# Kernel optimization log

Measured on AMD Instinct MI355X. Metric: run time of the kernel, lower is better.

The kernel has to match this reference:

```python
import jax, jax.numpy as jnp
import numpy as np


def setup_inputs() -> dict:
    key = jax.random.key(0)
    ks = jax.random.split(key, 9)
    N, C, SY, SX = 256, 128, 11, 25
    DM, DC, D = 64, 64, 128
    return {
        "f_t_global": jax.random.normal(ks[0], (N, D), dtype=jnp.float32),
        "x_t_local": jax.random.normal(ks[1], (N, C, SY, SX), dtype=jnp.float32),
        "x_t_prev_local": jax.random.normal(ks[2], (N, C, SY, SX), dtype=jnp.float32),
        "m_t": jax.random.normal(ks[3], (N, DM), dtype=jnp.float32),
        "m_t_prev": jax.random.normal(ks[4], (N, DM), dtype=jnp.float32),
        "c_t": jax.random.normal(ks[5], (N, DC), dtype=jnp.float32),
        "c_t_prev": jax.random.normal(ks[6], (N, DC), dtype=jnp.float32),
        "W_join": jax.random.normal(ks[7], (C + DM + DC, D), dtype=jnp.float32) * 0.05,
        "b_join": jax.random.normal(ks[8], (D,), dtype=jnp.float32) * 0.05,
    }


def reference(f_t_global, x_t_local, x_t_prev_local, m_t, m_t_prev, c_t, c_t_prev, W_join, b_join):
    N, C, SY, SX = x_t_local.shape
    P = SY * SX
    DM = m_t.shape[1]
    # join_obs(local, m, c) = concat([local, m, c]) @ W_join + b_join, split for efficiency
    Wl = W_join[:C]                 # [C, D]
    Wm = W_join[C:C + DM]           # [DM, D]
    Wc = W_join[C + DM:]            # [DC, D]
    # [N, C, SY, SX] -> [P, N, C]: all spatial positions batched at once
    loc_t = x_t_local.reshape(N, C, P).transpose(2, 0, 1)
    loc_p = x_t_prev_local.reshape(N, C, P).transpose(2, 0, 1)
    bias_t = m_t @ Wm + c_t @ Wc + b_join             # [N, D], shared across positions
    bias_p = m_t_prev @ Wm + c_t_prev @ Wc + b_join   # [N, D]
    positive = jnp.einsum('pnc,cd->pnd', loc_p, Wl) + bias_p[None]  # [P, N, D]
    pred_loc = jnp.einsum('pnc,cd->pnd', loc_t, Wl) + bias_t[None]  # [P, N, D]

    # loss1: global prediction vs per-position prev-local positives
    logits1 = jnp.einsum('nd,pmd->pnm', f_t_global, positive)   # [P, N, N]
    # loss2: per-position current-local vs per-position prev-local
    logits2 = jnp.einsum('pnd,pmd->pnm', pred_loc, positive)    # [P, N, N]

    def mean_infonce(logits):
        # cross_entropy(logits, arange(N)) averaged over batch, then over positions
        lse = jax.nn.logsumexp(logits, axis=-1)            # [P, N]
        diag = jnp.diagonal(logits, axis1=1, axis2=2)      # [P, N]
        return jnp.mean(lse - diag)

    loss1 = mean_infonce(logits1)
    loss2 = mean_infonce(logits2)
    return loss1 + loss2
```

## Files before the change

kernel.cpp:

```cpp
#include <hip/hip_runtime.h>

#define Nn 256
#define Cc 128
#define Pp 275
#define Dd 128

typedef unsigned int u32;
typedef unsigned short u16;
typedef float f32x4 __attribute__((ext_vector_type(4)));
typedef short bf16x8 __attribute__((ext_vector_type(8)));

__device__ __forceinline__ float bf2f(u16 h) {
    return __uint_as_float(((u32)h) << 16);
}
__device__ __forceinline__ u16 f2bf(float f) {
    u32 u = __float_as_uint(f);
    return (u16)((u + 0x7fffu + ((u >> 16) & 1u)) >> 16);
}

__global__ __launch_bounds__(256) void bias_kernel(
    const float* __restrict__ m_t, const float* __restrict__ m_p,
    const float* __restrict__ c_t, const float* __restrict__ c_p,
    const float* __restrict__ W, const float* __restrict__ b,
    const float* __restrict__ f,
    float* __restrict__ bias_t, float* __restrict__ bias_p,
    u16* __restrict__ f_bf, u16* __restrict__ WlT)
{
    int idx = blockIdx.x * 256 + threadIdx.x;
    int n = idx >> 7, d = idx & 127;
    float at = 0.f, ap = 0.f;
#pragma unroll 8
    for (int k = 0; k < 64; ++k) {
        float wm = W[(128 + k) * 128 + d];
        float wc = W[(192 + k) * 128 + d];
        at = fmaf(m_t[n * 64 + k], wm, at);
        at = fmaf(c_t[n * 64 + k], wc, at);
        ap = fmaf(m_p[n * 64 + k], wm, ap);
        ap = fmaf(c_p[n * 64 + k], wc, ap);
    }
    float bb = b[d];
    bias_t[idx] = at + bb;
    bias_p[idx] = ap + bb;
    f_bf[idx] = f2bf(f[idx]);
    if (idx < 16384) {
        int dd = idx >> 7, cc = idx & 127;
        WlT[idx] = f2bf(W[cc * 128 + dd]);
    }
}

__global__ __launch_bounds__(512) void join_full_kernel(
    const float* __restrict__ x_t, const float* __restrict__ x_p,
    const u16* __restrict__ WlT,
    const float* __restrict__ bias_t, const float* __restrict__ bias_p,
    u16* __restrict__ pred, u16* __restrict__ pos)
{
    __shared__ u16 xlds[275 * 128];
    const int tid = threadIdx.x;
    const int pass = blockIdx.x;
    const int n = blockIdx.y;
    const int w = tid >> 6;
    const int l = tid & 63;
    const int g = l >> 4;

    const float* sx = (pass ? x_p : x_t) + (size_t)n * (Cc * Pp);
    u16* outp = pass ? pos : pred;

    bf16x8 B[4];
    {
        const int row = w * 16 + (l & 15);
#pragma unroll
        for (int kk = 0; kk < 4; ++kk)
            B[kk] = *reinterpret_cast<const bf16x8*>(
                (const char*)WlT + row * 256 + kk * 64 + g * 16);
    }
    const float bv = (pass ? bias_p : bias_t)[n * 128 + w * 16 + (l & 15)];

    {
        const int c0 = (tid >> 3) * 2;
        const int j = tid & 7;
        const float* r0p = sx + (size_t)c0 * Pp;
        const float* r1p = r0p + Pp;

        f32x4 v0[9], v1[9];
#pragma unroll
        for (int i = 0; i < 9; ++i) {
            const int q = j + 8 * i;
            if (q < 68) {
                v0[i] = *reinterpret_cast<const f32x4*>(r0p + 4 * q);
                v1[i] = *reinterpret_cast<const f32x4*>(r1p + 4 * q);
            } else if (q == 68) {
                f32x4 a, c;
#pragma unroll
                for (int e = 0; e < 4; ++e) {
                    int pe = 4 * 68 + e; if (pe > Pp - 1) pe = Pp - 1;
                    a[e] = r0p[pe]; c[e] = r1p[pe];
                }
                v0[i] = a; v1[i] = c;
            }
        }
        asm volatile("" ::: "memory");
#pragma unroll
        for (int i = 0; i < 9; ++i) {
            const int q = j + 8 * i;
            if (q < 69) {
#pragma unroll
                for (int e = 0; e < 4; ++e) {
                    int p = 4 * q + e; if (p > Pp - 1) p = Pp - 1;
                    const int col = (c0 * 2) ^ ((p & 7) << 4) ^ (((p >> 3) & 1) << 5);
                    *reinterpret_cast<u32*>((char*)xlds + p * 256 + col) =
                        (u32)f2bf(v0[i][e]) | ((u32)f2bf(v1[i][e]) << 16);
                }
            }
        }
    }
    __syncthreads();

    const int d = w * 16 + (l & 15);
#pragma unroll
    for (int t = 0; t < 18; ++t) {
        const int p0 = (t < 17) ? t * 16 : 259;
        const int arow = p0 + (l & 15);
        bf16x8 A[4];
#pragma unroll
        for (int kk = 0; kk < 4; ++kk) {
            const int col = (kk * 64 + g * 16) ^ ((arow & 7) << 4) ^ (((arow >> 3) & 1) << 5);
            A[kk] = *reinterpret_cast<const bf16x8*>((const char*)xlds + arow * 256 + col);
        }
        f32x4 acc = {0.f, 0.f, 0.f, 0.f};
#pragma unroll
        for (int kk = 0; kk < 4; ++kk)
            acc = __builtin_amdgcn_mfma_f32_16x16x32_bf16(A[kk], B[kk], acc, 0, 0, 0);
#pragma unroll
        for (int r = 0; r < 4; ++r) {
            const int p = p0 + g * 4 + r;
            outp[((size_t)p * Nn + n) * Dd + d] = f2bf(acc[r] + bv);
        }
    }
}

__global__ __launch_bounds__(512) void logits_part_kernel(
    const u16* __restrict__ f_bf,
    const u16* __restrict__ pred, const u16* __restrict__ pos,
    float* __restrict__ spart, float* __restrict__ dgarr)
{
    __shared__ u16 lds[128 * Dd];
    const int tid = threadIdx.x;
    const int sel = blockIdx.x >> 1;
    const int mhalf = blockIdx.x & 1;
    const int p = blockIdx.y;
    const int w = tid >> 6;
    const int l = tid & 63;
    const int r0 = w * 32;

    {
        const uint4* src = reinterpret_cast<const uint4*>(
            pos + (size_t)p * (Nn * Dd) + (size_t)mhalf * 128 * Dd);
#pragma unroll
        for (int it = 0; it < 4; ++it) {
            int j = tid + 512 * it;
            int row = j >> 4;
            int colb = (j & 15) << 4;
            uint4 v = src[j];
            *reinterpret_cast<uint4*>((char*)lds + row * 256 + (colb ^ ((row & 7) << 4))) = v;
        }
    }

    const u16* Abase = sel ? (pred + (size_t)p * (Nn * Dd)) : f_bf;
    bf16x8 A[2][4];
    {
        const int arow = l & 15;
        const int acol = (l >> 4) << 4;
#pragma unroll
        for (int rt = 0; rt < 2; ++rt)
#pragma unroll
            for (int kk = 0; kk < 4; ++kk) {
                const char* ap = (const char*)Abase
                               + (size_t)(r0 + rt * 16 + arow) * 256 + kk * 64 + acol;
                A[rt][kk] = *reinterpret_cast<const bf16x8*>(ap);
            }
    }

    __syncthreads();

    const float L2E = 1.4426950408889634f;
    float s_[2][4];
    float dg[2][4];
#pragma unroll
    for (int rt = 0; rt < 2; ++rt)
#pragma unroll
        for (int r = 0; r < 4; ++r) { s_[rt][r] = 0.f; dg[rt][r] = 0.f; }

    const int mcol = l & 15;
    const int bcol = (l >> 4) << 4;

    for (int ctl = 0; ctl < 8; ++ctl) {
        bf16x8 B[4];
        const int mrow = ctl * 16 + mcol;
#pragma unroll
        for (int kk = 0; kk < 4; ++kk) {
            int cb = kk * 64 + bcol;
            B[kk] = *reinterpret_cast<const bf16x8*>(
                (const char*)lds + mrow * 256 + (cb ^ ((mrow & 7) << 4)));
        }
#pragma unroll
        for (int rt = 0; rt < 2; ++rt) {
            f32x4 acc = {0.f, 0.f, 0.f, 0.f};
#pragma unroll
            for (int kk = 0; kk < 4; ++kk)
                acc = __builtin_amdgcn_mfma_f32_16x16x32_bf16(A[rt][kk], B[kk], acc, 0, 0, 0);
            const bool isdg_ct = ((mhalf * 8 + ctl) == ((r0 >> 4) + rt));
#pragma unroll
            for (int r = 0; r < 4; ++r) {
                float v = acc[r];
                s_[rt][r] += __builtin_amdgcn_exp2f(fmaf(v, L2E, -64.f));
                if (isdg_ct && ((l & 15) == (((l >> 4) << 2) + r))) dg[rt][r] = v;
            }
        }
    }

    float* sp = spart + (((size_t)(sel * Pp + p) * 2 + mhalf) << 8);
    float* dp = dgarr + (((size_t)(sel * Pp + p)) << 8);
    const bool owns_dg = ((w >> 2) == mhalf);
#pragma unroll
    for (int rt = 0; rt < 2; ++rt)
#pragma unroll
        for (int r = 0; r < 4; ++r) {
            float s = s_[rt][r];
            s += __shfl_xor(s, 1);
            s += __shfl_xor(s, 2);
            s += __shfl_xor(s, 4);
            s += __shfl_xor(s, 8);
            if ((l & 15) == (((l >> 4) << 2) + r)) {
                const int nn = r0 + rt * 16 + ((l >> 4) << 2) + r;
                sp[nn] = s;
                if (owns_dg) dp[nn] = dg[rt][r];
            }
        }
}

__global__ __launch_bounds__(256) void merge_kernel(
    const float* __restrict__ spart, const float* __restrict__ dgarr,
    float* __restrict__ partial)
{
    __shared__ float red[256];
    const int sel = blockIdx.x;
    const int p = blockIdx.y;
    const int n = threadIdx.x;
    const size_t base = ((size_t)(sel * Pp + p) * 2) << 8;
    float s = spart[base + n] + spart[base + 256 + n];
    float dgv = dgarr[(((size_t)(sel * Pp + p)) << 8) + n];
    float val = 0.6931471805599453f * (64.f + __log2f(s)) - dgv;
    red[n] = val;
    __syncthreads();
    for (int k = 128; k > 0; k >>= 1) {
        if (n < k) red[n] += red[n + k];
        __syncthreads();
    }
    if (n == 0) partial[sel * Pp + p] = red[0];
}

__global__ __launch_bounds__(256) void reduce_kernel(
    const float* __restrict__ partial, float* __restrict__ out)
{
    __shared__ float red[256];
    float s = 0.f;
    for (int i = threadIdx.x; i < 2 * Pp; i += 256) s += partial[i];
    red[threadIdx.x] = s;
    __syncthreads();
    for (int k = 128; k > 0; k >>= 1) {
        if (threadIdx.x < k) red[threadIdx.x] += red[threadIdx.x + k];
        __syncthreads();
    }
    if (threadIdx.x == 0) out[0] = red[0] * (1.0f / (Pp * (float)Nn));
}

extern "C" void kernel_launch(void* const* d_in, const int* in_sizes, int n_in,
                              void* d_out, int out_size, void* d_ws, size_t ws_size,
                              hipStream_t stream)
{
    const float* f   = (const float*)d_in[0];
    const float* x_t = (const float*)d_in[1];
    const float* x_p = (const float*)d_in[2];
    const float* m_t = (const float*)d_in[3];
    const float* m_p = (const float*)d_in[4];
    const float* c_t = (const float*)d_in[5];
    const float* c_p = (const float*)d_in[6];
    const float* W   = (const float*)d_in[7];
    const float* b   = (const float*)d_in[8];

    char* ws = (char*)d_ws;
    const size_t SLAB = (size_t)Pp * Nn * Dd;

    float* bias_t = (float*)ws;
    float* bias_p = bias_t + Nn * Dd;
    u16* f_bf = (u16*)(ws + 262144);
    u16* WlT  = f_bf + Nn * Dd;
    u16* pred = (u16*)(ws + 360448);
    u16* pos  = pred + SLAB;
    float* partial = (float*)(pos + SLAB);
    float* spart   = partial + 2 * Pp;
    float* dgarr   = spart + (size_t)2 * Pp * 2 * 256;

    bias_kernel<<<dim3(Nn * Dd / 256), 256, 0, stream>>>(m_t, m_p, c_t, c_p, W, b, f,
                                                         bias_t, bias_p, f_bf, WlT);
    join_full_kernel<<<dim3(2, Nn), 512, 0, stream>>>(x_t, x_p, WlT, bias_t, bias_p,
                                                      pred, pos);
    logits_part_kernel<<<dim3(4, Pp), 512, 0, stream>>>(f_bf, pred, pos, spart, dgarr);
    merge_kernel<<<dim3(2, Pp), 256, 0, stream>>>(spart, dgarr, partial);
    reduce_kernel<<<1, 256, 0, stream>>>(partial, (float*)d_out);
}
```

Measured before the change: 62.20 us.

## Split join kernel input staging into two halves to overlap loads with MFMA

The join kernel now stages the spatial positions in two LDS halves (144 and 131 positions). It issues the global loads for the second half into registers before running the MFMA tiles on the first half, so memory latency hides behind compute. LDS use stays about the same (two buffers of 144 rows) while register pressure rises from holding the prefetched second half. It also adds a second barrier.

```diff
diff --git a/kernel.cpp b/kernel.cpp
--- a/kernel.cpp
+++ b/kernel.cpp
@@ -48,13 +48,13 @@
     }
 }
 
-__global__ __launch_bounds__(512) void join_full_kernel(
+__global__ __launch_bounds__(512) void join_dbuf2_kernel(
     const float* __restrict__ x_t, const float* __restrict__ x_p,
     const u16* __restrict__ WlT,
     const float* __restrict__ bias_t, const float* __restrict__ bias_p,
     u16* __restrict__ pred, u16* __restrict__ pos)
 {
-    __shared__ u16 xlds[275 * 128];
+    __shared__ u16 xlds[2][144 * 128];
     const int tid = threadIdx.x;
     const int pass = blockIdx.x;
     const int n = blockIdx.y;
@@ -75,39 +75,32 @@
     }
     const float bv = (pass ? bias_p : bias_t)[n * 128 + w * 16 + (l & 15)];
 
+    const int c0 = (tid >> 3) * 2;
+    const int j = tid & 7;
+    const float* r0p = sx + (size_t)c0 * Pp;
+    const float* r1p = r0p + Pp;
+    const int d = w * 16 + (l & 15);
+
     {
-        const int c0 = (tid >> 3) * 2;
-        const int j = tid & 7;
-        const float* r0p = sx + (size_t)c0 * Pp;
-        const float* r1p = r0p + Pp;
-
-        f32x4 v0[9], v1[9];
-#pragma unroll
-        for (int i = 0; i < 9; ++i) {
+        f32x4 v0[5], v1[5];
+#pragma unroll
+        for (int i = 0; i < 5; ++i) {
             const int q = j + 8 * i;
-            if (q < 68) {
+            if (q < 36) {
                 v0[i] = *reinterpret_cast<const f32x4*>(r0p + 4 * q);
                 v1[i] = *reinterpret_cast<const f32x4*>(r1p + 4 * q);
-            } else if (q == 68) {
-                f32x4 a, c;
+            }
+        }
+        asm volatile("" ::: "memory");
+#pragma unroll
+        for (int i = 0; i < 5; ++i) {
+            const int q = j + 8 * i;
+            if (q < 36) {
 #pragma unroll
                 for (int e = 0; e < 4; ++e) {
-                    int pe = 4 * 68 + e; if (pe > Pp - 1) pe = Pp - 1;
-                    a[e] = r0p[pe]; c[e] = r1p[pe];
-                }
-                v0[i] = a; v1[i] = c;
-            }
-        }
-        asm volatile("" ::: "memory");
-#pragma unroll
-        for (int i = 0; i < 9; ++i) {
-            const int q = j + 8 * i;
-            if (q < 69) {
-#pragma unroll
-                for (int e = 0; e < 4; ++e) {
-                    int p = 4 * q + e; if (p > Pp - 1) p = Pp - 1;
-                    const int col = (c0 * 2) ^ ((p & 7) << 4) ^ (((p >> 3) & 1) << 5);
-                    *reinterpret_cast<u32*>((char*)xlds + p * 256 + col) =
+                    const int lp = 4 * q + e;
+                    const int col = (c0 * 2) ^ ((lp & 7) << 4) ^ (((lp >> 3) & 1) << 5);
+                    *reinterpret_cast<u32*>((char*)&xlds[0][0] + lp * 256 + col) =
                         (u32)f2bf(v0[i][e]) | ((u32)f2bf(v1[i][e]) << 16);
                 }
             }
@@ -115,16 +108,70 @@
     }
     __syncthreads();
 
-    const int d = w * 16 + (l & 15);
-#pragma unroll
-    for (int t = 0; t < 18; ++t) {
+    f32x4 u0[5], u1[5];
+#pragma unroll
+    for (int i = 0; i < 5; ++i) {
+        const int q = j + 8 * i;
+        if (q < 32) {
+            u0[i] = *reinterpret_cast<const f32x4*>(r0p + 144 + 4 * q);
+            u1[i] = *reinterpret_cast<const f32x4*>(r1p + 144 + 4 * q);
+        } else if (q == 32) {
+            f32x4 a, c;
+#pragma unroll
+            for (int e = 0; e < 4; ++e) {
+                int pe = 144 + 128 + e; if (pe > Pp - 1) pe = Pp - 1;
+                a[e] = r0p[pe]; c[e] = r1p[pe];
+            }
+            u0[i] = a; u1[i] = c;
+        }
+    }
+    asm volatile("" ::: "memory");
+
+#pragma unroll
+    for (int t = 0; t < 9; ++t) {
+        const int p0 = t * 16;
+        const int lrow = p0 + (l & 15);
+        bf16x8 A[4];
+#pragma unroll
+        for (int kk = 0; kk < 4; ++kk) {
+            const int col = (kk * 64 + g * 16) ^ ((lrow & 7) << 4) ^ (((lrow >> 3) & 1) << 5);
+            A[kk] = *reinterpret_cast<const bf16x8*>((const char*)&xlds[0][0] + lrow * 256 + col);
+        }
+        f32x4 acc = {0.f, 0.f, 0.f, 0.f};
+#pragma unroll
+        for (int kk = 0; kk < 4; ++kk)
+            acc = __builtin_amdgcn_mfma_f32_16x16x32_bf16(A[kk], B[kk], acc, 0, 0, 0);
+#pragma unroll
+        for (int r = 0; r < 4; ++r) {
+            const int p = p0 + g * 4 + r;
+            outp[((size_t)p * Nn + n) * Dd + d] = f2bf(acc[r] + bv);
+        }
+    }
+
+#pragma unroll
+    for (int i = 0; i < 5; ++i) {
+        const int q = j + 8 * i;
+        if (q < 33) {
+#pragma unroll
+            for (int e = 0; e < 4; ++e) {
+                const int lp = 4 * q + e;
+                const int col = (c0 * 2) ^ ((lp & 7) << 4) ^ (((lp >> 3) & 1) << 5);
+                *reinterpret_cast<u32*>((char*)&xlds[1][0] + lp * 256 + col) =
+                    (u32)f2bf(u0[i][e]) | ((u32)f2bf(u1[i][e]) << 16);
+            }
+        }
+    }
+    __syncthreads();
+
+#pragma unroll
+    for (int t = 9; t < 18; ++t) {
         const int p0 = (t < 17) ? t * 16 : 259;
-        const int arow = p0 + (l & 15);
+        const int lrow = p0 - 144 + (l & 15);
         bf16x8 A[4];
 #pragma unroll
         for (int kk = 0; kk < 4; ++kk) {
-            const int col = (kk * 64 + g * 16) ^ ((arow & 7) << 4) ^ (((arow >> 3) & 1) << 5);
-            A[kk] = *reinterpret_cast<const bf16x8*>((const char*)xlds + arow * 256 + col);
+            const int col = (kk * 64 + g * 16) ^ ((lrow & 7) << 4) ^ (((lrow >> 3) & 1) << 5);
+            A[kk] = *reinterpret_cast<const bf16x8*>((const char*)&xlds[1][0] + lrow * 256 + col);
         }
         f32x4 acc = {0.f, 0.f, 0.f, 0.f};
 #pragma unroll
@@ -303,8 +350,8 @@
 
     bias_kernel<<<dim3(Nn * Dd / 256), 256, 0, stream>>>(m_t, m_p, c_t, c_p, W, b, f,
                                                          bias_t, bias_p, f_bf, WlT);
-    join_full_kernel<<<dim3(2, Nn), 512, 0, stream>>>(x_t, x_p, WlT, bias_t, bias_p,
-                                                      pred, pos);
+    join_dbuf2_kernel<<<dim3(2, Nn), 512, 0, stream>>>(x_t, x_p, WlT, bias_t, bias_p,
+                                                       pred, pos);
     logits_part_kernel<<<dim3(4, Pp), 512, 0, stream>>>(f_bf, pred, pos, spart, dgarr);
     merge_kernel<<<dim3(2, Pp), 256, 0, stream>>>(spart, dgarr, partial);
     reduce_kernel<<<1, 256, 0, stream>>>(partial, (float*)d_out);
```

After: 65.92 us. +6.0%, slower.
